# Kernel tuning notes

Measured on AMD Instinct MI355X. Metric: run time of the kernel, lower is better.

Reference implementation:

```python
import jax, jax.numpy as jnp
import numpy as np

N_CRYST = 64
ATOMS_PER = 32
N = N_CRYST * ATOMS_PER          # 2048 atoms
NBR = 20                         # max_neighbors
E = N * NBR                      # 40960 edges
C = 128                          # sphere_channels(_reduce)
HID = 256                        # hidden_channels
NB = 128                         # num_basis_functions
NLAYER = 8                       # num_interactions
LMAX = 6
K = 1 + 3 * LMAX                 # SH coeffs with mmax=1 -> 19
MAXZ = 100                       # MAX_ATOMIC_NUM
ZDIM = 256
CUT = 8.0
FOUR_PI = 4.0 * np.pi


def sph_harm_m01(d):
    """Real spherical harmonics Y_l^m, l<=LMAX, m in {-1,0,1}. d: [E,3] unit vecs -> [E,K]."""
    x, y, ct = d[:, 0], d[:, 1], d[:, 2]
    rho = jnp.sqrt(x * x + y * y) + 1e-12   # sin(theta)
    cph, sph = x / rho, y / rho
    # Legendre P_l(ct)
    P0 = [jnp.ones_like(ct), ct]
    for l in range(2, LMAX + 1):
        P0.append(((2 * l - 1) * ct * P0[l - 1] - (l - 1) * P0[l - 2]) / l)
    # Associated Legendre P_l^1(ct)
    P1 = {1: -rho, 2: -3.0 * ct * rho}
    for l in range(3, LMAX + 1):
        P1[l] = ((2 * l - 1) * ct * P1[l - 1] - l * P1[l - 2]) / (l - 1)
    Ys = [jnp.full_like(ct, float(np.sqrt(1.0 / FOUR_PI)))]
    for l in range(1, LMAX + 1):
        K0 = float(np.sqrt((2 * l + 1) / FOUR_PI))
        K1 = float(np.sqrt(2.0 * (2 * l + 1) / FOUR_PI / (l * (l + 1))))
        Ys += [K1 * P1[l] * sph, K0 * P0[l], K1 * P1[l] * cph]  # m=-1,0,+1
    return jnp.stack(Ys, axis=-1)


def lattice_from_params(lengths, angles):
    """lengths,angles(deg): [B,3] -> lattice row-vectors [B,3,3]."""
    a, b, c = lengths[:, 0], lengths[:, 1], lengths[:, 2]
    rad = angles * (np.pi / 180.0)
    ca, cb, cg = jnp.cos(rad[:, 0]), jnp.cos(rad[:, 1]), jnp.cos(rad[:, 2])
    sg = jnp.sin(rad[:, 2])
    z0 = jnp.zeros_like(a)
    v3y = (ca - cb * cg) / sg
    v3z = jnp.sqrt(jnp.clip(1.0 - cb * cb - v3y * v3y, 1e-8))
    l1 = jnp.stack([a, z0, z0], -1)
    l2 = jnp.stack([b * cg, b * sg, z0], -1)
    l3 = jnp.stack([c * cb, c * v3y, c * v3z], -1)
    return jnp.stack([l1, l2, l3], axis=1)


def setup_inputs() -> dict:
    key = jax.random.key(0)
    ks = jax.random.split(key, 16)
    z = jax.random.normal(ks[0], (N_CRYST, ZDIM), jnp.float32)
    frac = jax.random.uniform(ks[1], (N, 3), jnp.float32)
    atom_types = jax.random.randint(ks[2], (N,), 1, MAXZ + 1)
    num_atoms = jnp.full((N_CRYST,), ATOMS_PER, jnp.int32)
    lengths = 4.0 + 4.0 * jax.random.uniform(ks[3], (N_CRYST, 3), jnp.float32)
    angles = 80.0 + 20.0 * jax.random.uniform(ks[4], (N_CRYST, 3), jnp.float32)
    batch = jnp.arange(N) // ATOMS_PER
    # NBR incoming edges per atom, sources restricted to the same crystal
    dst = jnp.repeat(jnp.arange(N), NBR)
    src_local = jax.random.randint(ks[5], (E,), 0, ATOMS_PER)
    src = (dst // ATOMS_PER) * ATOMS_PER + src_local
    edge_index = jnp.stack([src, dst], axis=0)
    sc = lambda k, sh, fan: jax.random.normal(k, sh, jnp.float32) / np.sqrt(fan)
    params = dict(
        emb=sc(ks[6], (MAXZ + 1, C), 1.0),
        zproj=sc(ks[7], (ZDIM, C), ZDIM),
        Wd=sc(ks[8], (NLAYER, NB, HID), NB),
        W1=sc(ks[9], (NLAYER, C, HID), C),
        W2=sc(ks[10], (NLAYER, HID, C), HID),
        Wa=sc(ks[11], (C, MAXZ), C),
        ba=jnp.zeros((MAXZ,), jnp.float32),
        wf=sc(ks[12], (C,), C),
    )
    return dict(z=z, pred_frac_coords=frac, pred_atom_types=atom_types,
                num_atoms=num_atoms, lengths=lengths, angles=angles,
                batch=batch, edge_index=edge_index, **params)


def reference(z, pred_frac_coords, pred_atom_types, num_atoms, lengths, angles,
              batch, edge_index, emb, zproj, Wd, W1, W2, Wa, ba, wf):
    lat = lattice_from_params(lengths, angles)                 # [B,3,3]
    pos = jnp.einsum('ni,nij->nj', pred_frac_coords, lat[batch])  # [N,3]
    src, dst = edge_index[0], edge_index[1]
    vec = pos[src] - pos[dst]                                  # [E,3]
    dist = jnp.linalg.norm(vec, axis=-1) + 1e-8
    dirn = vec / dist[:, None]
    offsets = jnp.linspace(0.0, CUT, NB)
    width = offsets[1] - offsets[0]
    rbf = jnp.exp(-0.5 * ((dist[:, None] - offsets) / width) ** 2)  # [E,NB]
    Y = sph_harm_m01(dirn)                                     # [E,K]
    # node SH features, l=0 initialized from atom embedding + latent
    x = jnp.zeros((N, K, C), pred_frac_coords.dtype)
    x = x.at[:, 0, :].set(emb[pred_atom_types] + (z @ zproj)[batch])
    for l in range(NLAYER):
        s = jnp.einsum('ek,ekc->ec', Y, x[src])                # project along edge frame
        h = jax.nn.silu(s @ W1[l] + rbf @ Wd[l])               # [E,HID]
        m = h @ W2[l]                                          # [E,C]
        agg = jax.ops.segment_sum(Y[:, :, None] * m[:, None, :], dst, num_segments=N)
        x = x + agg / NBR
    h_node = x[:, 0, :]                                        # [N,C]
    atom_logits = h_node @ Wa + ba                             # [N,MAXZ]
    fscal = (h_node[src] - h_node[dst]) @ wf                   # [E]
    coord_diff = jax.ops.segment_sum(fscal[:, None] * dirn, dst, num_segments=N)
    return coord_diff, atom_logits
```

## Files before the change

kernel.cpp:

```cpp
#include <hip/hip_runtime.h>
#include <hip/hip_bf16.h>

#define N_CRYST 64
#define ATOMS_PER 32
#define NN 2048
#define NBRS 20
#define EE 40960
#define CC 128
#define HIDDIM 256
#define NBASIS 128
#define NLAYERS 8
#define LMAXV 6
#define KK 19
#define MAXZV 100
#define ZDIMV 256
#define FOUR_PI_F 12.566370614359172f

typedef unsigned short ushort_t;
typedef __attribute__((ext_vector_type(8))) short short8;
typedef __attribute__((ext_vector_type(4))) float floatx4;

__device__ __forceinline__ ushort_t f2us(float f) {
    union { float f; unsigned u; } x;
    x.f = f;
    unsigned r = (x.u + 0x7fffu + ((x.u >> 16) & 1u)) >> 16;
    return (ushort_t)r;
}
__device__ __forceinline__ float us2f(unsigned u) {
    return __uint_as_float(u << 16);
}

__global__ void k_geom(const float* __restrict__ frac, const float* __restrict__ lengths,
                       const float* __restrict__ angles, const int* __restrict__ ei,
                       float* __restrict__ dist, float* __restrict__ dirn,
                       float* __restrict__ Yv, int* __restrict__ trp,
                       int* __restrict__ tloc) {
    const int cr = blockIdx.x;
    const int t = threadIdx.x;
    __shared__ float posL[32][3];
    __shared__ int cnt[8][32], base[8][32];

    if (t < 32) {
        int n = cr * 32 + t;
        float la = lengths[cr * 3 + 0];
        float lb = lengths[cr * 3 + 1];
        float lc = lengths[cr * 3 + 2];
        const float D2R = 0.017453292519943295f;
        float aa = angles[cr * 3 + 0] * D2R;
        float ab = angles[cr * 3 + 1] * D2R;
        float ag = angles[cr * 3 + 2] * D2R;
        float ca = cosf(aa), cb = cosf(ab), cg = cosf(ag), sg = sinf(ag);
        float v3y = (ca - cb * cg) / sg;
        float v3z = sqrtf(fmaxf(1.0f - cb * cb - v3y * v3y, 1e-8f));
        float f0 = frac[n * 3 + 0];
        float f1 = frac[n * 3 + 1];
        float f2 = frac[n * 3 + 2];
        posL[t][0] = f0 * la + f1 * (lb * cg) + f2 * (lc * cb);
        posL[t][1] = f1 * (lb * sg) + f2 * (lc * v3y);
        posL[t][2] = f2 * (lc * v3z);
    }
    cnt[t >> 5][t & 31] = 0;
    __syncthreads();

    for (int j = t; j < 640; j += 256) {
        int e = cr * 640 + j;
        int s = ei[e] - cr * 32, d = ei[EE + e] - cr * 32;
        float vx = posL[s][0] - posL[d][0];
        float vy = posL[s][1] - posL[d][1];
        float vz = posL[s][2] - posL[d][2];
        float dd = sqrtf(vx * vx + vy * vy + vz * vz) + 1e-8f;
        float ix = vx / dd, iy = vy / dd, iz = vz / dd;
        dist[e] = dd;
        dirn[e * 3 + 0] = ix;
        dirn[e * 3 + 1] = iy;
        dirn[e * 3 + 2] = iz;

        float ct = iz;
        float rho = sqrtf(ix * ix + iy * iy) + 1e-12f;
        float cph = ix / rho, sph = iy / rho;
        float P0[LMAXV + 1], P1[LMAXV + 1];
        P0[0] = 1.0f;
        P0[1] = ct;
        #pragma unroll
        for (int l = 2; l <= LMAXV; l++)
            P0[l] = ((2 * l - 1) * ct * P0[l - 1] - (l - 1) * P0[l - 2]) / (float)l;
        P1[0] = 0.0f;
        P1[1] = -rho;
        P1[2] = -3.0f * ct * rho;
        #pragma unroll
        for (int l = 3; l <= LMAXV; l++)
            P1[l] = ((2 * l - 1) * ct * P1[l - 1] - l * P1[l - 2]) / (float)(l - 1);

        float* Ye = Yv + (size_t)e * KK;
        Ye[0] = 0.28209479177387814f;
        #pragma unroll
        for (int l = 1; l <= LMAXV; l++) {
            float K0 = sqrtf((2 * l + 1) / FOUR_PI_F);
            float K1 = sqrtf(2.0f * (2 * l + 1) / (FOUR_PI_F * l * (l + 1)));
            Ye[3 * l - 2] = K1 * P1[l] * sph;
            Ye[3 * l - 1] = K0 * P0[l];
            Ye[3 * l]     = K1 * P1[l] * cph;
        }
        atomicAdd(&cnt[j / 80][s], 1);
    }
    __syncthreads();

    if (t < 8) {
        int run = 0;
        for (int a = 0; a < 32; a++) {
            base[t][a] = run;
            trp[(cr * 8 + t) * 33 + a] = run;
            run += cnt[t][a];
        }
        trp[(cr * 8 + t) * 33 + 32] = run;
    }
    __syncthreads();
    cnt[t >> 5][t & 31] = 0;
    __syncthreads();
    for (int j = t; j < 640; j += 256) {
        int e = cr * 640 + j;
        int s = ei[e] - cr * 32;
        int tt = j / 80;
        int slot = base[tt][s] + atomicAdd(&cnt[tt][s], 1);
        tloc[(cr * 8 + tt) * 80 + slot] = j - tt * 80;
    }
}

__global__ void k_rbfA(const float* __restrict__ dist, ushort_t* __restrict__ Abf) {
    int idx = blockIdx.x * blockDim.x + threadIdx.x;
    if (idx >= EE * NBASIS) return;
    int e = idx >> 7, j = idx & 127;
    const float width = 8.0f / 127.0f;
    const float invw = 127.0f / 8.0f;
    float t = (dist[e] - (float)j * width) * invw;
    Abf[(size_t)e * 256 + 128 + j] = f2us(expf(-0.5f * t * t));
}

__global__ void k_wt(const float* __restrict__ W1, const float* __restrict__ Wd,
                     const float* __restrict__ W2,
                     ushort_t* __restrict__ WT1, ushort_t* __restrict__ WT2) {
    int idx = blockIdx.x * blockDim.x + threadIdx.x;
    const int n1 = NLAYERS * HIDDIM * 256;
    if (idx < n1) {
        int l = idx >> 16;
        int r = idx & 65535;
        int n = r >> 8, k = r & 255;
        float v = (k < 128) ? W1[((size_t)l * CC + k) * HIDDIM + n]
                            : Wd[((size_t)l * NBASIS + (k - 128)) * HIDDIM + n];
        WT1[idx] = f2us(v);
    } else {
        int j = idx - n1;
        if (j >= NLAYERS * CC * HIDDIM) return;
        int l = j >> 15;
        int r = j & 32767;
        int n = r >> 8, k = r & 255;
        WT2[j] = f2us(W2[((size_t)l * HIDDIM + k) * CC + n]);
    }
}

__global__ void k_xinit(const int* __restrict__ atype, const int* __restrict__ batch,
                        const float* __restrict__ emb, const float* __restrict__ z,
                        const float* __restrict__ zproj, ushort_t* __restrict__ xbf) {
    int idx = blockIdx.x * blockDim.x + threadIdx.x;
    if (idx >= NN * KK * CC) return;
    int n = idx / (KK * CC);
    int r = idx - n * (KK * CC);
    float v = 0.0f;
    if (r < CC) {
        v = emb[atype[n] * CC + r];
        const float* zb = z + (size_t)batch[n] * ZDIMV;
        for (int d = 0; d < ZDIMV; d++) v += zb[d] * zproj[d * CC + r];
    }
    xbf[idx] = f2us(v);
}

__global__ __launch_bounds__(512, 2) void k_layer(const int* __restrict__ trp,
                                                  const int* __restrict__ tloc,
                                                  const float* __restrict__ Yv,
                                                  const ushort_t* __restrict__ Abf,
                                                  const ushort_t* __restrict__ WT1,
                                                  const ushort_t* __restrict__ WT2,
                                                  const ushort_t* __restrict__ xbfin,
                                                  ushort_t* __restrict__ xbfout) {
    __shared__ char smraw[47360];
    ushort_t* As  = (ushort_t*)smraw;
    ushort_t* Hs  = (ushort_t*)smraw;
    ushort_t* Ms  = (ushort_t*)smraw;
    float*   Ylds = (float*)(smraw + 40960);

    const int t = threadIdx.x;
    const int bid = ((blockIdx.x & 7) << 6) | (blockIdx.x >> 3);
    const int w = t >> 6, lane = t & 63;
    const int quad = lane >> 4, lrow = lane & 15;
    const int e0 = bid * 80;
    const int cr = bid >> 3;

    const float* Yb = Yv + (size_t)e0 * KK;
    #pragma unroll
    for (int j = 0; j < 3; j++) {
        int i = t + j * 512;
        if (i < 80 * KK) Ylds[(i / KK) * 20 + (i % KK)] = Yb[i];
    }
    if (t < 80) Ylds[t * 20 + 19] = 0.f;
    __syncthreads();

    short8 arg[3];
    #pragma unroll
    for (int i = 0; i < 3; i++) {
        int idx = i * 512 + t;
        if (idx < 1280) {
            int r = idx >> 4, g16 = idx & 15;
            arg[i] = *(const short8*)(Abf + (size_t)(e0 + r) * 256 + 128 + g16 * 8);
        }
    }

    const int c2 = lane * 2;
    const int sgrp = lane >> 2;
    const int soff = (lane & 3) * 2;
    #pragma unroll 1
    for (int a8 = 0; a8 < 4; a8++) {
        const int a = w * 4 + a8;
        const int i0 = trp[bid * 33 + a];
        const int i1 = trp[bid * 33 + a + 1];
        if (i0 == i1) continue;
        const ushort_t* xsrc = xbfin + (size_t)(cr * 32 + a) * (KK * CC) + c2;
        float2 xr[KK];
        #pragma unroll
        for (int k = 0; k < KK; k++) {
            unsigned u = *(const unsigned*)(xsrc + k * CC);
            xr[k] = make_float2(us2f(u & 0xffffu), us2f(u >> 16));
        }
        for (int i = i0; i < i1; i++) {
            const int r = tloc[bid * 80 + i];
            const float* yp = Ylds + r * 20;
            float ax = 0.f, ay = 0.f;
            #pragma unroll
            for (int k = 0; k < KK; k++) {
                float y = yp[k];
                ax += y * xr[k].x;
                ay += y * xr[k].y;
            }
            unsigned pk = (unsigned)f2us(ax) | (((unsigned)f2us(ay)) << 16);
            *(unsigned*)&As[r * 256 + ((sgrp ^ (r & 7)) << 3) + soff] = pk;
        }
    }

    #pragma unroll
    for (int i = 0; i < 3; i++) {
        int idx = i * 512 + t;
        if (idx < 1280) {
            int r = idx >> 4, g = 16 + (idx & 15);
            *(short8*)&As[r * 256 + ((g ^ (r & 7)) << 3)] = arg[i];
        }
    }

    const ushort_t* W1w = WT1 + (size_t)(w * 32) * 256;
    short8 bp0[2], bp1[2];
    #pragma unroll
    for (int ni = 0; ni < 2; ni++) {
        bp0[ni] = *(const short8*)(W1w + (size_t)(ni * 16 + lrow) * 256 + quad * 8);
        bp1[ni] = *(const short8*)(W1w + (size_t)(ni * 16 + lrow) * 256 + 32 + quad * 8);
    }
    __syncthreads();

    floatx4 acc[5][2];
    #pragma unroll
    for (int mi = 0; mi < 5; mi++)
        #pragma unroll
        for (int ni = 0; ni < 2; ni++) acc[mi][ni] = (floatx4){0.f, 0.f, 0.f, 0.f};

    #pragma unroll
    for (int s8 = 0; s8 < 8; s8++) {
        short8 bcur[2];
        if (s8 & 1) {
            #pragma unroll
            for (int ni = 0; ni < 2; ni++) bcur[ni] = bp1[ni];
            if (s8 < 6) {
                const int kn = (s8 + 2) * 32 + quad * 8;
                #pragma unroll
                for (int ni = 0; ni < 2; ni++)
                    bp1[ni] = *(const short8*)(W1w + (size_t)(ni * 16 + lrow) * 256 + kn);
            }
        } else {
            #pragma unroll
            for (int ni = 0; ni < 2; ni++) bcur[ni] = bp0[ni];
            if (s8 < 6) {
                const int kn = (s8 + 2) * 32 + quad * 8;
                #pragma unroll
                for (int ni = 0; ni < 2; ni++)
                    bp0[ni] = *(const short8*)(W1w + (size_t)(ni * 16 + lrow) * 256 + kn);
            }
        }
        const int grp = s8 * 4 + quad;
        short8 af[5];
        #pragma unroll
        for (int mi = 0; mi < 5; mi++) {
            const int r = mi * 16 + lrow;
            af[mi] = *(const short8*)&As[r * 256 + ((grp ^ (r & 7)) << 3)];
        }
        __builtin_amdgcn_s_setprio(1);
        #pragma unroll
        for (int ni = 0; ni < 2; ni++)
            #pragma unroll
            for (int mi = 0; mi < 5; mi++)
                acc[mi][ni] = __builtin_amdgcn_mfma_f32_16x16x32_bf16(
                    af[mi], bcur[ni], acc[mi][ni], 0, 0, 0);
        __builtin_amdgcn_s_setprio(0);
    }

    const ushort_t* W2w = WT2 + (size_t)(w * 16) * 256;
    short8 bq0, bq1;
    bq0 = *(const short8*)(W2w + (size_t)lrow * 256 + quad * 8);
    bq1 = *(const short8*)(W2w + (size_t)lrow * 256 + 32 + quad * 8);
    __syncthreads();

    #pragma unroll
    for (int mi = 0; mi < 5; mi++) {
        const int row = mi * 16 + quad * 4;
        #pragma unroll
        for (int ni = 0; ni < 2; ni++) {
            const int col = w * 32 + ni * 16 + lrow;
            #pragma unroll
            for (int r = 0; r < 4; r++) {
                float v = acc[mi][ni][r];
                v = v * __builtin_amdgcn_rcpf(1.0f + __expf(-v));
                const int rr = row + r;
                Hs[rr * 256 + ((((col >> 3) ^ (rr & 7)) << 3) | (col & 7))] = f2us(v);
            }
        }
    }
    __syncthreads();

    floatx4 macc[5];
    #pragma unroll
    for (int mi = 0; mi < 5; mi++) macc[mi] = (floatx4){0.f, 0.f, 0.f, 0.f};

    #pragma unroll
    for (int s8 = 0; s8 < 8; s8++) {
        short8 bcur;
        if (s8 & 1) {
            bcur = bq1;
            if (s8 < 6) {
                const int kn = (s8 + 2) * 32 + quad * 8;
                bq1 = *(const short8*)(W2w + (size_t)lrow * 256 + kn);
            }
        } else {
            bcur = bq0;
            if (s8 < 6) {
                const int kn = (s8 + 2) * 32 + quad * 8;
                bq0 = *(const short8*)(W2w + (size_t)lrow * 256 + kn);
            }
        }
        const int grp = s8 * 4 + quad;
        short8 af[5];
        #pragma unroll
        for (int mi = 0; mi < 5; mi++) {
            const int r = mi * 16 + lrow;
            af[mi] = *(const short8*)&Hs[r * 256 + ((grp ^ (r & 7)) << 3)];
        }
        __builtin_amdgcn_s_setprio(1);
        #pragma unroll
        for (int mi = 0; mi < 5; mi++)
            macc[mi] = __builtin_amdgcn_mfma_f32_16x16x32_bf16(
                af[mi], bcur, macc[mi], 0, 0, 0);
        __builtin_amdgcn_s_setprio(0);
    }
    __syncthreads();

    #pragma unroll
    for (int mi = 0; mi < 5; mi++) {
        const int row = mi * 16 + quad * 4;
        const int col = w * 16 + lrow;
        #pragma unroll
        for (int r = 0; r < 4; r++)
            Ms[(row + r) * 132 + col] = f2us(macc[mi][r]);
    }
    __syncthreads();

    const int node = t >> 7;
    const int cq = t & 127;
    const int ng = bid * 4 + node;
    const ushort_t* xbi = xbfin + (size_t)ng * (KK * CC) + cq;
    ushort_t* xbo = xbfout + (size_t)ng * (KK * CC) + cq;

    float xold[KK];
    #pragma unroll
    for (int k = 0; k < KK; k++) xold[k] = us2f((unsigned)xbi[k * CC]);

    float xacc[KK];
    #pragma unroll
    for (int k = 0; k < KK; k++) xacc[k] = 0.f;

    #pragma unroll 4
    for (int e = 0; e < NBRS; e++) {
        const int eg = node * NBRS + e;
        const float m0 = us2f((unsigned)Ms[eg * 132 + cq]);
        const float* yp = Ylds + eg * 20;
        #pragma unroll
        for (int kq = 0; kq < 5; kq++) {
            float4 y = *(const float4*)(yp + kq * 4);
            const int k = kq * 4;
            xacc[k + 0] += y.x * m0;
            xacc[k + 1] += y.y * m0;
            xacc[k + 2] += y.z * m0;
            if (kq < 4) xacc[k + 3] += y.w * m0;
        }
    }
    const float s = 1.0f / (float)NBRS;
    #pragma unroll
    for (int k = 0; k < KK; k++) {
        float nv = xold[k] + xacc[k] * s;
        xbo[k * CC] = f2us(nv);
    }
}

#define COORD_BLKS 512
__global__ void k_head(const int* __restrict__ ei, const ushort_t* __restrict__ xbf,
                       const float* __restrict__ wf, const float* __restrict__ dirn,
                       const float* __restrict__ Wa, const float* __restrict__ ba,
                       float* __restrict__ out) {
    const int bid = blockIdx.x;
    const int t = threadIdx.x;
    if (bid < COORD_BLKS) {
        __shared__ float fs[4][NBRS];
        __shared__ float wsh[CC];
        const int g = t >> 6, lane = t & 63;
        const int n = bid * 4 + g;
        if (t < CC) wsh[t] = wf[t];
        __syncthreads();
        if (lane < NBRS) {
            int e = n * NBRS + lane;
            int sidx = ei[e];
            const ushort_t* xs = xbf + (size_t)sidx * (KK * CC);
            const ushort_t* xd = xbf + (size_t)n * (KK * CC);
            float acc = 0.0f;
            for (int c = 0; c < CC; c++)
                acc += (us2f((unsigned)xs[c]) - us2f((unsigned)xd[c])) * wsh[c];
            fs[g][lane] = acc;
        }
        __syncthreads();
        if (lane < 3) {
            float acc = 0.0f;
            #pragma unroll
            for (int j = 0; j < NBRS; j++)
                acc += fs[g][j] * dirn[(size_t)(n * NBRS + j) * 3 + lane];
            out[n * 3 + lane] = acc;
        }
    } else {
        int idx = (bid - COORD_BLKS) * 256 + t;
        if (idx >= NN * MAXZV) return;
        int n = idx / MAXZV, a = idx - n * MAXZV;
        float acc = ba[a];
        const ushort_t* hn = xbf + (size_t)n * (KK * CC);
        for (int c = 0; c < CC; c++) acc += us2f((unsigned)hn[c]) * Wa[c * MAXZV + a];
        out[NN * 3 + idx] = acc;
    }
}

extern "C" void kernel_launch(void* const* d_in, const int* in_sizes, int n_in,
                              void* d_out, int out_size, void* d_ws, size_t ws_size,
                              hipStream_t stream) {
    (void)in_sizes; (void)n_in; (void)out_size; (void)ws_size;
    const float* z       = (const float*)d_in[0];
    const float* frac    = (const float*)d_in[1];
    const int*   atype   = (const int*)d_in[2];
    const float* lengths = (const float*)d_in[4];
    const float* angles  = (const float*)d_in[5];
    const int*   batch   = (const int*)d_in[6];
    const int*   ei      = (const int*)d_in[7];
    const float* emb     = (const float*)d_in[8];
    const float* zproj   = (const float*)d_in[9];
    const float* Wd      = (const float*)d_in[10];
    const float* W1      = (const float*)d_in[11];
    const float* W2      = (const float*)d_in[12];
    const float* Wa      = (const float*)d_in[13];
    const float* ba      = (const float*)d_in[14];
    const float* wf      = (const float*)d_in[15];
    float* out = (float*)d_out;

    float* ws = (float*)d_ws;
    float* dist = ws; ws += EE;
    float* dirn = ws; ws += EE * 3;
    float* Yv   = ws; ws += (size_t)EE * KK + 4;
    ushort_t* xbfA = (ushort_t*)ws; ws += (size_t)NN * KK * CC / 2;
    ushort_t* xbfB = (ushort_t*)ws; ws += (size_t)NN * KK * CC / 2;
    int* trp  = (int*)ws;
    int* tloc = trp + 512 * 33;
    ushort_t* Abf  = (ushort_t*)(tloc + 512 * 80);
    ushort_t* WT1  = Abf + (size_t)EE * 256;
    ushort_t* WT2  = WT1 + (size_t)NLAYERS * 256 * 256;

    k_geom<<<N_CRYST, 256, 0, stream>>>(frac, lengths, angles, ei, dist, dirn, Yv, trp, tloc);
    k_rbfA<<<(EE * NBASIS) / 256, 256, 0, stream>>>(dist, Abf);
    k_wt<<<(NLAYERS * (HIDDIM * 256 + CC * HIDDIM)) / 256, 256, 0, stream>>>(W1, Wd, W2, WT1, WT2);
    k_xinit<<<(NN * KK * CC) / 256, 256, 0, stream>>>(atype, batch, emb, z, zproj, xbfA);

    for (int l = 0; l < NLAYERS; l++) {
        const ushort_t* xbi = (l & 1) ? xbfB : xbfA;
        ushort_t*       xbo = (l & 1) ? xbfA : xbfB;
        k_layer<<<512, 512, 0, stream>>>(trp, tloc, Yv, Abf,
                                         WT1 + (size_t)l * 256 * 256,
                                         WT2 + (size_t)l * CC * HIDDIM,
                                         xbi, xbo);
    }

    k_head<<<COORD_BLKS + (NN * MAXZV) / 256, 256, 0, stream>>>(ei, xbfA, wf, dirn,
                                                                Wa, ba, out);
}
```

Baseline: 435.5 us.

## Fuse preprocessing kernels and hoist latent projection per crystal

```diff
diff --git a/kernel.cpp b/kernel.cpp
--- a/kernel.cpp
+++ b/kernel.cpp
@@ -32,9 +32,10 @@
 
 __global__ void k_geom(const float* __restrict__ frac, const float* __restrict__ lengths,
                        const float* __restrict__ angles, const int* __restrict__ ei,
+                       const float* __restrict__ z, const float* __restrict__ zproj,
                        float* __restrict__ dist, float* __restrict__ dirn,
                        float* __restrict__ Yv, int* __restrict__ trp,
-                       int* __restrict__ tloc) {
+                       int* __restrict__ tloc, float* __restrict__ zc) {
     const int cr = blockIdx.x;
     const int t = threadIdx.x;
     __shared__ float posL[32][3];
@@ -124,54 +125,73 @@
         int slot = base[tt][s] + atomicAdd(&cnt[tt][s], 1);
         tloc[(cr * 8 + tt) * 80 + slot] = j - tt * 80;
     }
-}
-
-__global__ void k_rbfA(const float* __restrict__ dist, ushort_t* __restrict__ Abf) {
-    int idx = blockIdx.x * blockDim.x + threadIdx.x;
-    if (idx >= EE * NBASIS) return;
-    int e = idx >> 7, j = idx & 127;
-    const float width = 8.0f / 127.0f;
-    const float invw = 127.0f / 8.0f;
-    float t = (dist[e] - (float)j * width) * invw;
-    Abf[(size_t)e * 256 + 128 + j] = f2us(expf(-0.5f * t * t));
-}
-
-__global__ void k_wt(const float* __restrict__ W1, const float* __restrict__ Wd,
-                     const float* __restrict__ W2,
-                     ushort_t* __restrict__ WT1, ushort_t* __restrict__ WT2) {
-    int idx = blockIdx.x * blockDim.x + threadIdx.x;
-    const int n1 = NLAYERS * HIDDIM * 256;
-    if (idx < n1) {
-        int l = idx >> 16;
-        int r = idx & 65535;
-        int n = r >> 8, k = r & 255;
-        float v = (k < 128) ? W1[((size_t)l * CC + k) * HIDDIM + n]
-                            : Wd[((size_t)l * NBASIS + (k - 128)) * HIDDIM + n];
-        WT1[idx] = f2us(v);
+
+    if (t < CC) {
+        float acc = 0.f;
+        const float* zb = z + (size_t)cr * ZDIMV;
+        for (int d = 0; d < ZDIMV; d++) acc += zb[d] * zproj[d * CC + t];
+        zc[cr * CC + t] = acc;
+    }
+}
+
+#define WT_BLKS 3072
+#define RBF_BLKS 2560
+#define XI_BLKS 4864
+__global__ void k_prep(const float* __restrict__ W1, const float* __restrict__ Wd,
+                       const float* __restrict__ W2,
+                       ushort_t* __restrict__ WT1, ushort_t* __restrict__ WT2,
+                       const float* __restrict__ dist, ushort_t* __restrict__ Abf,
+                       const int* __restrict__ atype, const int* __restrict__ batch,
+                       const float* __restrict__ emb, const float* __restrict__ zc,
+                       ushort_t* __restrict__ xbf) {
+    const int bid = blockIdx.x;
+    const int t = threadIdx.x;
+    if (bid < WT_BLKS) {
+        int idx = bid * 256 + t;
+        const int n1 = NLAYERS * HIDDIM * 256;
+        if (idx < n1) {
+            int l = idx >> 16;
+            int r = idx & 65535;
+            int n = r >> 8, k = r & 255;
+            float v = (k < 128) ? W1[((size_t)l * CC + k) * HIDDIM + n]
+                                : Wd[((size_t)l * NBASIS + (k - 128)) * HIDDIM + n];
+            WT1[idx] = f2us(v);
+        } else {
+            int j = idx - n1;
+            int l = j >> 15;
+            int r = j & 32767;
+            int n = r >> 8, k = r & 255;
+            WT2[j] = f2us(W2[((size_t)l * HIDDIM + k) * CC + n]);
+        }
+    } else if (bid < WT_BLKS + RBF_BLKS) {
+        int idx = (bid - WT_BLKS) * 256 + t;
+        int e = idx >> 4, j8 = (idx & 15) * 8;
+        const float width = 8.0f / 127.0f;
+        const float invw = 127.0f / 8.0f;
+        float dd = dist[e];
+        short8 v;
+        #pragma unroll
+        for (int jj = 0; jj < 8; jj++) {
+            float x = (dd - (float)(j8 + jj) * width) * invw;
+            ((ushort_t*)&v)[jj] = f2us(__expf(-0.5f * x * x));
+        }
+        *(short8*)&Abf[(size_t)e * 256 + 128 + j8] = v;
     } else {
-        int j = idx - n1;
-        if (j >= NLAYERS * CC * HIDDIM) return;
-        int l = j >> 15;
-        int r = j & 32767;
-        int n = r >> 8, k = r & 255;
-        WT2[j] = f2us(W2[((size_t)l * HIDDIM + k) * CC + n]);
-    }
-}
-
-__global__ void k_xinit(const int* __restrict__ atype, const int* __restrict__ batch,
-                        const float* __restrict__ emb, const float* __restrict__ z,
-                        const float* __restrict__ zproj, ushort_t* __restrict__ xbf) {
-    int idx = blockIdx.x * blockDim.x + threadIdx.x;
-    if (idx >= NN * KK * CC) return;
-    int n = idx / (KK * CC);
-    int r = idx - n * (KK * CC);
-    float v = 0.0f;
-    if (r < CC) {
-        v = emb[atype[n] * CC + r];
-        const float* zb = z + (size_t)batch[n] * ZDIMV;
-        for (int d = 0; d < ZDIMV; d++) v += zb[d] * zproj[d * CC + r];
-    }
-    xbf[idx] = f2us(v);
+        int idx4 = (bid - WT_BLKS - RBF_BLKS) * 256 + t;
+        int basei = idx4 * 4;
+        if (basei >= NN * KK * CC) return;
+        int n = basei / (KK * CC);
+        int r = basei - n * (KK * CC);
+        ushort_t v4[4];
+        #pragma unroll
+        for (int j = 0; j < 4; j++) {
+            int rr = r + j;
+            float v = 0.f;
+            if (rr < CC) v = emb[atype[n] * CC + rr] + zc[batch[n] * CC + rr];
+            v4[j] = f2us(v);
+        }
+        *(uint2*)&xbf[basei] = *(uint2*)v4;
+    }
 }
 
 __global__ __launch_bounds__(512, 2) void k_layer(const int* __restrict__ trp,
@@ -482,6 +502,7 @@
     float* dist = ws; ws += EE;
     float* dirn = ws; ws += EE * 3;
     float* Yv   = ws; ws += (size_t)EE * KK + 4;
+    float* zc   = ws; ws += N_CRYST * CC;
     ushort_t* xbfA = (ushort_t*)ws; ws += (size_t)NN * KK * CC / 2;
     ushort_t* xbfB = (ushort_t*)ws; ws += (size_t)NN * KK * CC / 2;
     int* trp  = (int*)ws;
@@ -490,10 +511,11 @@
     ushort_t* WT1  = Abf + (size_t)EE * 256;
     ushort_t* WT2  = WT1 + (size_t)NLAYERS * 256 * 256;
 
-    k_geom<<<N_CRYST, 256, 0, stream>>>(frac, lengths, angles, ei, dist, dirn, Yv, trp, tloc);
-    k_rbfA<<<(EE * NBASIS) / 256, 256, 0, stream>>>(dist, Abf);
-    k_wt<<<(NLAYERS * (HIDDIM * 256 + CC * HIDDIM)) / 256, 256, 0, stream>>>(W1, Wd, W2, WT1, WT2);
-    k_xinit<<<(NN * KK * CC) / 256, 256, 0, stream>>>(atype, batch, emb, z, zproj, xbfA);
+    k_geom<<<N_CRYST, 256, 0, stream>>>(frac, lengths, angles, ei, z, zproj,
+                                        dist, dirn, Yv, trp, tloc, zc);
+    k_prep<<<WT_BLKS + RBF_BLKS + XI_BLKS, 256, 0, stream>>>(W1, Wd, W2, WT1, WT2,
+                                                             dist, Abf, atype, batch,
+                                                             emb, zc, xbfA);
 
     for (int l = 0; l < NLAYERS; l++) {
         const ushort_t* xbi = (l & 1) ? xbfB : xbfA;
```

Measured after the change: 411.5 us, median of 3. 1.06x faster.
